# Kernel optimization log

Measured on AMD Instinct MI355X. Metric: run time of the kernel, lower is better.

The kernel has to match this reference:

```python
import jax, jax.numpy as jnp
import numpy as np

N_NODES = 100000
N_EDGES = 1600000
IN_DIM = 128
HIDDEN = 128


def setup_inputs() -> dict:
    key = jax.random.key(0)
    k1, k2, k3 = jax.random.split(key, 3)
    x = jax.random.normal(k1, (N_NODES, IN_DIM), dtype=jnp.float32)
    edge_index = jax.random.randint(k2, (2, N_EDGES), 0, N_NODES, dtype=jnp.int64)
    # Glorot-ish init for the GCN weight
    W = jax.random.normal(k3, (IN_DIM, HIDDEN), dtype=jnp.float32) * (1.0 / np.sqrt(IN_DIM))
    b = jnp.zeros((HIDDEN,), dtype=jnp.float32)
    return {"x": x, "edge_index": edge_index, "W": W, "b": b}


def reference(x, edge_index, W, b):
    N = x.shape[0]
    # PyG GCNConv: add self-loops, symmetric deg^{-1/2} normalization,
    # linear transform, scatter-add aggregation at destination, + bias.
    loop = jnp.arange(N, dtype=edge_index.dtype)
    src = jnp.concatenate([edge_index[0], loop])
    dst = jnp.concatenate([edge_index[1], loop])

    ones = jnp.ones(src.shape[0], dtype=x.dtype)
    deg = jax.ops.segment_sum(ones, dst, num_segments=N)  # in-degree incl. self-loop
    dinv = jnp.where(deg > 0, jax.lax.rsqrt(deg), 0.0)
    norm = dinv[src] * dinv[dst]  # [E+N]

    xw = x @ W  # [N, H] dense transform first (GCNConv default)
    msgs = xw[src] * norm[:, None]  # gather + scale, [E+N, H]
    out = jax.ops.segment_sum(msgs, dst, num_segments=N) + b  # scatter-add
    return jax.nn.relu(out)
```

## Files before the change

kernel.cpp:

```cpp
#include <hip/hip_runtime.h>
#include <hip/hip_bf16.h>


#define NP1 512
#define MAXB 1024

typedef short  short8 __attribute__((ext_vector_type(8)));
typedef float  f32x4  __attribute__((ext_vector_type(4)));

__device__ inline unsigned short f2b(float f) {
    unsigned u = __float_as_uint(f);
    return (unsigned short)((u + 0x7fffu + ((u >> 16) & 1u)) >> 16);
}

__device__ inline void acc4(float4& a, unsigned lo, unsigned hi) {
    a.x += __uint_as_float(lo << 16);
    a.y += __uint_as_float(lo & 0xffff0000u);
    a.z += __uint_as_float(hi << 16);
    a.w += __uint_as_float(hi & 0xffff0000u);
}

__global__ __launch_bounds__(256) void k_hist(const int* __restrict__ dst,
                                              int* __restrict__ hist,
                                              const float* __restrict__ W,
                                              unsigned short* __restrict__ Wt,
                                              int E, int B, int chunk) {
    __shared__ int h[MAXB];
    for (int i = threadIdx.x; i < B; i += 256) h[i] = 0;
    __syncthreads();
    int e0 = blockIdx.x * chunk;
    int e1 = min(E, e0 + chunk);
    for (int e = e0 + threadIdx.x; e < e1; e += 256)
        atomicAdd(&h[dst[e] >> 7], 1);
    __syncthreads();
    for (int i = threadIdx.x; i < B; i += 256)
        hist[i * NP1 + blockIdx.x] = h[i];
    if (blockIdx.x < 64) {
        int i = blockIdx.x * 256 + threadIdx.x;
        int k = i >> 7, n = i & 127;
        Wt[n * 128 + k] = f2b(W[k * 128 + n]);
    }
}

__global__ __launch_bounds__(256) void k_scanrow(int* __restrict__ hist,
                                                 int* __restrict__ btotal, int B) {
    __shared__ int s[256];
    const int b = blockIdx.x;
    const int t = threadIdx.x;
    int v0 = hist[b * NP1 + 2 * t];
    int v1 = hist[b * NP1 + 2 * t + 1];
    int pair = v0 + v1;
    s[t] = pair;
    __syncthreads();
    for (int off = 1; off < 256; off <<= 1) {
        int add = (t >= off) ? s[t - off] : 0;
        __syncthreads();
        s[t] += add;
        __syncthreads();
    }
    int exc = s[t] - pair;
    hist[b * NP1 + 2 * t]     = exc;
    hist[b * NP1 + 2 * t + 1] = exc + v0;
    if (t == 255) btotal[b] = s[255];
}

__global__ __launch_bounds__(256) void k_scanb(const int* __restrict__ btotal,
                                               int* __restrict__ bbase, int B) {
    __shared__ int s[256];
    const int t = threadIdx.x;
    int v[4];
    int loc = 0;
#pragma unroll
    for (int k = 0; k < 4; ++k) {
        int idx = t * 4 + k;
        v[k] = (idx < B) ? btotal[idx] : 0;
        loc += v[k];
    }
    s[t] = loc;
    __syncthreads();
    for (int off = 1; off < 256; off <<= 1) {
        int add = (t >= off) ? s[t - off] : 0;
        __syncthreads();
        s[t] += add;
        __syncthreads();
    }
    int run = s[t] - loc;
#pragma unroll
    for (int k = 0; k < 4; ++k) {
        int idx = t * 4 + k;
        if (idx < B) bbase[idx] = run;
        run += v[k];
    }
}

__global__ __launch_bounds__(256) void k_scatter(const int* __restrict__ src,
                                                 const int* __restrict__ dst,
                                                 const int* __restrict__ hist,
                                                 const int* __restrict__ bbase,
                                                 unsigned* __restrict__ bucketed,
                                                 int E, int B, int chunk) {
    __shared__ int cur[MAXB];
    for (int i = threadIdx.x; i < B; i += 256)
        cur[i] = bbase[i] + hist[i * NP1 + blockIdx.x];
    __syncthreads();
    int e0 = blockIdx.x * chunk;
    int e1 = min(E, e0 + chunk);
    for (int e = e0 + threadIdx.x; e < e1; e += 256) {
        int d = dst[e];
        int p = atomicAdd(&cur[d >> 7], 1);
        bucketed[p] = (unsigned)src[e] | ((unsigned)(d & 127) << 17);
    }
}

__global__ __launch_bounds__(256) void k_csr(const unsigned* __restrict__ bucketed,
                                             const int* __restrict__ bbase,
                                             const int* __restrict__ btotal,
                                             int* __restrict__ csr_src,
                                             int* __restrict__ rowptr,
                                             float* __restrict__ dinv_g,
                                             int E, int B, int N) {
    const int b = blockIdx.x;
    const int t = threadIdx.x;
    const int base = bbase[b];
    const int cnt = btotal[b];
    const int node0 = b << 7;

    __shared__ int sdeg[128], sscan[128], cur[128];
    if (t < 128) sdeg[t] = 0;
    __syncthreads();
    for (int i = t; i < cnt; i += 256)
        atomicAdd(&sdeg[bucketed[base + i] >> 17], 1);
    __syncthreads();
    if (t < 128) sscan[t] = sdeg[t];
    __syncthreads();
    for (int off = 1; off < 128; off <<= 1) {
        int add = 0;
        if (t < 128 && t >= off) add = sscan[t - off];
        __syncthreads();
        if (t < 128) sscan[t] += add;
        __syncthreads();
    }
    if (t < 128) {
        int rs = sscan[t] - sdeg[t];
        cur[t] = rs;
        int node = node0 + t;
        if (node < N) {
            rowptr[node] = base + rs;
            dinv_g[node] = rsqrtf((float)(sdeg[t] + 1));
        }
    }
    if (b == B - 1 && t == 0) rowptr[N] = E;
    __syncthreads();
    for (int i = t; i < cnt; i += 256) {
        unsigned w = bucketed[base + i];
        int p = atomicAdd(&cur[w >> 17], 1);
        csr_src[base + p] = (int)(w & 0x1FFFFu);
    }
}

__global__ __launch_bounds__(256) void k_gemm(const float* __restrict__ x,
                                              const unsigned short* __restrict__ Wt,
                                              const float* __restrict__ dinv,
                                              unsigned* __restrict__ xs_out,
                                              int N, int row_base) {
    __shared__ short out_lds[4][16][136];
    const int t = threadIdx.x;
    const int wv = t >> 6;
    const int lane = t & 63;
    const int quad = lane >> 4;
    const int lid = lane & 15;
    const int row0 = row_base + blockIdx.x * 64;

    int grow = row0 + wv * 16 + lid;
    int growc = grow < N ? grow : N - 1;
    short8 af[4];
#pragma unroll
    for (int q = 0; q < 4; ++q) {
        const float4* xr = (const float4*)(x + (size_t)growc * 128 + q * 32 + quad * 8);
        float4 f0 = xr[0], f1 = xr[1];
        af[q][0] = (short)f2b(f0.x); af[q][1] = (short)f2b(f0.y);
        af[q][2] = (short)f2b(f0.z); af[q][3] = (short)f2b(f0.w);
        af[q][4] = (short)f2b(f1.x); af[q][5] = (short)f2b(f1.y);
        af[q][6] = (short)f2b(f1.z); af[q][7] = (short)f2b(f1.w);
    }

    int drow = row0 + wv * 16 + quad * 4;
    float4 dv4;
    if (drow + 3 < N)      dv4 = *(const float4*)(dinv + drow);
    else {
        dv4.x = dinv[min(drow + 0, N - 1)];
        dv4.y = dinv[min(drow + 1, N - 1)];
        dv4.z = dinv[min(drow + 2, N - 1)];
        dv4.w = dinv[min(drow + 3, N - 1)];
    }

#pragma unroll
    for (int c = 0; c < 8; ++c) {
        f32x4 acc = {0.f, 0.f, 0.f, 0.f};
#pragma unroll
        for (int q = 0; q < 4; ++q) {
            const short8* bp = (const short8*)(Wt + (size_t)(c * 16 + lid) * 128 +
                                               q * 32 + quad * 8);
            acc = __builtin_amdgcn_mfma_f32_16x16x32_bf16(af[q], *bp, acc, 0, 0, 0);
        }
        out_lds[wv][quad * 4 + 0][c * 16 + lid] = (short)f2b(acc[0] * dv4.x);
        out_lds[wv][quad * 4 + 1][c * 16 + lid] = (short)f2b(acc[1] * dv4.y);
        out_lds[wv][quad * 4 + 2][c * 16 + lid] = (short)f2b(acc[2] * dv4.z);
        out_lds[wv][quad * 4 + 3][c * 16 + lid] = (short)f2b(acc[3] * dv4.w);
    }
    __syncthreads();

    int rl = lane >> 2;
    int cseg = lane & 3;
    int grow2 = row0 + wv * 16 + rl;
    if (grow2 <= N) {
        uint4* dstp = (uint4*)(xs_out + (size_t)grow2 * 64);
        if (grow2 < N) {
            const uint4* srcp = (const uint4*)((const char*)&out_lds[wv][rl][0] + cseg * 64);
#pragma unroll
            for (int tt = 0; tt < 4; ++tt) dstp[cseg * 4 + tt] = srcp[tt];
        } else {
            uint4 z = make_uint4(0u, 0u, 0u, 0u);
#pragma unroll
            for (int tt = 0; tt < 4; ++tt) dstp[cseg * 4 + tt] = z;
        }
    }
}

__global__ __launch_bounds__(256) void k_aggregate(const uint4* __restrict__ xs4,
                                                   const int* __restrict__ csr_src,
                                                   const int* __restrict__ rowptr,
                                                   const float* __restrict__ dinv,
                                                   const float* __restrict__ bias,
                                                   float* __restrict__ out,
                                                   int N, int n_begin, int n_end) {
    const int t = threadIdx.x;
    const int lane = t & 63;
    const int sub = lane & 15;
    const int gbase = lane & 48;
    const int n = n_begin + blockIdx.x * 16 + (t >> 4);
    if (n >= n_end) return;

    const int rs = rowptr[n];
    const int re = rowptr[n + 1];
    const float dv = dinv[n];
    const char* xb = (const char*)xs4;
    const unsigned subo = (unsigned)sub << 4;

    float4 a0 = make_float4(0.f, 0.f, 0.f, 0.f);
    float4 a1 = make_float4(0.f, 0.f, 0.f, 0.f);

    int idx = N;
    if (rs + sub < re) idx = csr_src[rs + sub];

    for (int i0 = rs; i0 < re; i0 += 16) {
        const int idx_cur = idx;
        const int i1 = i0 + 16;
        idx = N;
        if (i1 + sub < re) idx = csr_src[i1 + sub];
        int m = re - i0; if (m > 16) m = 16;

        {
            int r0 = __shfl(idx_cur, gbase + 0);
            int r1 = __shfl(idx_cur, gbase + 1);
            int r2 = __shfl(idx_cur, gbase + 2);
            int r3 = __shfl(idx_cur, gbase + 3);
            int r4 = __shfl(idx_cur, gbase + 4);
            int r5 = __shfl(idx_cur, gbase + 5);
            int r6 = __shfl(idx_cur, gbase + 6);
            int r7 = __shfl(idx_cur, gbase + 7);
            uint4 u0 = *(const uint4*)(xb + ((((unsigned)r0) << 8) | subo));
            uint4 u1 = *(const uint4*)(xb + ((((unsigned)r1) << 8) | subo));
            uint4 u2 = *(const uint4*)(xb + ((((unsigned)r2) << 8) | subo));
            uint4 u3 = *(const uint4*)(xb + ((((unsigned)r3) << 8) | subo));
            uint4 u4 = *(const uint4*)(xb + ((((unsigned)r4) << 8) | subo));
            uint4 u5 = *(const uint4*)(xb + ((((unsigned)r5) << 8) | subo));
            uint4 u6 = *(const uint4*)(xb + ((((unsigned)r6) << 8) | subo));
            uint4 u7 = *(const uint4*)(xb + ((((unsigned)r7) << 8) | subo));
            acc4(a0, u0.x, u0.y); acc4(a1, u0.z, u0.w);
            acc4(a0, u1.x, u1.y); acc4(a1, u1.z, u1.w);
            acc4(a0, u2.x, u2.y); acc4(a1, u2.z, u2.w);
            acc4(a0, u3.x, u3.y); acc4(a1, u3.z, u3.w);
            acc4(a0, u4.x, u4.y); acc4(a1, u4.z, u4.w);
            acc4(a0, u5.x, u5.y); acc4(a1, u5.z, u5.w);
            acc4(a0, u6.x, u6.y); acc4(a1, u6.z, u6.w);
            acc4(a0, u7.x, u7.y); acc4(a1, u7.z, u7.w);
        }
        if (m > 8) {
            int r0 = __shfl(idx_cur, gbase + 8);
            int r1 = __shfl(idx_cur, gbase + 9);
            int r2 = __shfl(idx_cur, gbase + 10);
            int r3 = __shfl(idx_cur, gbase + 11);
            int r4 = __shfl(idx_cur, gbase + 12);
            int r5 = __shfl(idx_cur, gbase + 13);
            int r6 = __shfl(idx_cur, gbase + 14);
            int r7 = __shfl(idx_cur, gbase + 15);
            uint4 u0 = *(const uint4*)(xb + ((((unsigned)r0) << 8) | subo));
            uint4 u1 = *(const uint4*)(xb + ((((unsigned)r1) << 8) | subo));
            uint4 u2 = *(const uint4*)(xb + ((((unsigned)r2) << 8) | subo));
            uint4 u3 = *(const uint4*)(xb + ((((unsigned)r3) << 8) | subo));
            uint4 u4 = *(const uint4*)(xb + ((((unsigned)r4) << 8) | subo));
            uint4 u5 = *(const uint4*)(xb + ((((unsigned)r5) << 8) | subo));
            uint4 u6 = *(const uint4*)(xb + ((((unsigned)r6) << 8) | subo));
            uint4 u7 = *(const uint4*)(xb + ((((unsigned)r7) << 8) | subo));
            acc4(a0, u0.x, u0.y); acc4(a1, u0.z, u0.w);
            acc4(a0, u1.x, u1.y); acc4(a1, u1.z, u1.w);
            acc4(a0, u2.x, u2.y); acc4(a1, u2.z, u2.w);
            acc4(a0, u3.x, u3.y); acc4(a1, u3.z, u3.w);
            acc4(a0, u4.x, u4.y); acc4(a1, u4.z, u4.w);
            acc4(a0, u5.x, u5.y); acc4(a1, u5.z, u5.w);
            acc4(a0, u6.x, u6.y); acc4(a1, u6.z, u6.w);
            acc4(a0, u7.x, u7.y); acc4(a1, u7.z, u7.w);
        }
    }

    uint4 su = *(const uint4*)(xb + ((((unsigned)n) << 8) | subo));
    acc4(a0, su.x, su.y);
    acc4(a1, su.z, su.w);

    const float4* bp = (const float4*)bias;
    float4 b0 = bp[sub * 2];
    float4 b1 = bp[sub * 2 + 1];
    f32x4 o0, o1;
    o0[0] = fmaxf(dv * a0.x + b0.x, 0.f);
    o0[1] = fmaxf(dv * a0.y + b0.y, 0.f);
    o0[2] = fmaxf(dv * a0.z + b0.z, 0.f);
    o0[3] = fmaxf(dv * a0.w + b0.w, 0.f);
    o1[0] = fmaxf(dv * a1.x + b1.x, 0.f);
    o1[1] = fmaxf(dv * a1.y + b1.y, 0.f);
    o1[2] = fmaxf(dv * a1.z + b1.z, 0.f);
    o1[3] = fmaxf(dv * a1.w + b1.w, 0.f);

    f32x4* op = (f32x4*)(out + (size_t)n * 128 + sub * 8);
    __builtin_nontemporal_store(o0, op);
    __builtin_nontemporal_store(o1, op + 1);
}

extern "C" void kernel_launch(void* const* d_in, const int* in_sizes, int n_in,
                              void* d_out, int out_size, void* d_ws, size_t ws_size,
                              hipStream_t stream) {
    const float* x   = (const float*)d_in[0];
    const int*   ei  = (const int*)d_in[1];
    const float* W   = (const float*)d_in[2];
    const float* b   = (const float*)d_in[3];
    float*       out = (float*)d_out;

    const int N = in_sizes[0] / 128;
    const int E = in_sizes[1] / 2;
    const int* src = ei;
    const int* dst = ei + E;

    const int B = (N + 127) >> 7;
    const int M = B * NP1;
    const int chunk = (E + NP1 - 1) / NP1;

    auto align = [](size_t v) { return (v + 255) & ~(size_t)255; };
    char* p = (char*)d_ws;
    int*            hist     = (int*)p;            p += align((size_t)M * 4);
    int*            btotal   = (int*)p;            p += align((size_t)B * 4);
    int*            bbase    = (int*)p;            p += align((size_t)B * 4);
    int*            rowptr   = (int*)p;            p += align(((size_t)N + 1) * 4);
    float*          dinv     = (float*)p;          p += align((size_t)N * 4);
    unsigned*       bucketed = (unsigned*)p;       p += align((size_t)E * 4);
    int*            csr_src  = (int*)p;            p += align((size_t)E * 4);
    unsigned*       xs       = (unsigned*)p;       p += align(((size_t)N + 1) * 64 * 4);
    unsigned short* Wt       = (unsigned short*)p; p += align(128 * 128 * 2);
    (void)ws_size;

    k_hist    <<<NP1, 256, 0, stream>>>(dst, hist, W, Wt, E, B, chunk);
    k_scanrow <<<B, 256, 0, stream>>>(hist, btotal, B);
    k_scanb   <<<1, 256, 0, stream>>>(btotal, bbase, B);
    k_scatter <<<NP1, 256, 0, stream>>>(src, dst, hist, bbase, bucketed, E, B, chunk);
    k_csr     <<<B, 256, 0, stream>>>(bucketed, bbase, btotal, csr_src, rowptr,
                                      dinv, E, B, N);

    const int half = ((N / 2) + 63) / 64 * 64;
    const int g1 = half / 64;
    const int g2 = (N + 1 - half + 63) / 64;
    k_gemm <<<g1, 256, 0, stream>>>(x, Wt, dinv, xs, N, 0);
    k_gemm <<<g2, 256, 0, stream>>>(x, Wt, dinv, xs, N, half);

    const int q = (N + 3) / 4;
    for (int i = 0; i < 4; ++i) {
        int n0 = i * q;
        int n1 = min(N, n0 + q);
        if (n0 >= n1) break;
        int blocks = (n1 - n0 + 15) / 16;
        k_aggregate<<<blocks, 256, 0, stream>>>((const uint4*)xs, csr_src, rowptr,
                                                dinv, b, out, N, n0, n1);
    }
}
```

Baseline: 258.7 us.

## Fold bucket-base scan into scatter/csr, widen buckets, merge gemm and aggregate launches

Removes the single-block bucket-total scan kernel and recomputes the bucket base prefix inside k_scatter and k_csr, so there is one fewer launch and dependency step. Bucket width grows from 128 to 256 nodes per bucket, which halves the bucket count and gives larger k_csr blocks. The two gemm launches become one, and the aggregate launches drop from four to two, cutting launch overhead. The cost is that every scatter and csr block now repeats a redundant 256-wide scan, and the 256-node buckets mean fewer csr blocks with more per-bucket LDS atomics.

```diff
diff --git a/kernel.cpp b/kernel.cpp
--- a/kernel.cpp
+++ b/kernel.cpp
@@ -3,7 +3,8 @@
 
 
 #define NP1 512
-#define MAXB 1024
+#define BSH 8
+#define MAXB 512
 
 typedef short  short8 __attribute__((ext_vector_type(8)));
 typedef float  f32x4  __attribute__((ext_vector_type(4)));
@@ -31,7 +32,7 @@
     int e0 = blockIdx.x * chunk;
     int e1 = min(E, e0 + chunk);
     for (int e = e0 + threadIdx.x; e < e1; e += 256)
-        atomicAdd(&h[dst[e] >> 7], 1);
+        atomicAdd(&h[dst[e] >> BSH], 1);
     __syncthreads();
     for (int i = threadIdx.x; i < B; i += 256)
         hist[i * NP1 + blockIdx.x] = h[i];
@@ -64,56 +65,41 @@
     if (t == 255) btotal[b] = s[255];
 }
 
-__global__ __launch_bounds__(256) void k_scanb(const int* __restrict__ btotal,
-                                               int* __restrict__ bbase, int B) {
-    __shared__ int s[256];
-    const int t = threadIdx.x;
-    int v[4];
-    int loc = 0;
-#pragma unroll
-    for (int k = 0; k < 4; ++k) {
-        int idx = t * 4 + k;
-        v[k] = (idx < B) ? btotal[idx] : 0;
-        loc += v[k];
-    }
-    s[t] = loc;
-    __syncthreads();
-    for (int off = 1; off < 256; off <<= 1) {
-        int add = (t >= off) ? s[t - off] : 0;
-        __syncthreads();
-        s[t] += add;
-        __syncthreads();
-    }
-    int run = s[t] - loc;
-#pragma unroll
-    for (int k = 0; k < 4; ++k) {
-        int idx = t * 4 + k;
-        if (idx < B) bbase[idx] = run;
-        run += v[k];
-    }
-}
-
 __global__ __launch_bounds__(256) void k_scatter(const int* __restrict__ src,
                                                  const int* __restrict__ dst,
                                                  const int* __restrict__ hist,
-                                                 const int* __restrict__ bbase,
+                                                 const int* __restrict__ btotal,
                                                  unsigned* __restrict__ bucketed,
                                                  int E, int B, int chunk) {
     __shared__ int cur[MAXB];
-    for (int i = threadIdx.x; i < B; i += 256)
-        cur[i] = bbase[i] + hist[i * NP1 + blockIdx.x];
-    __syncthreads();
-    int e0 = blockIdx.x * chunk;
+    __shared__ int s[256];
+    const int t = threadIdx.x;
+    const int g = blockIdx.x;
+    int a0 = (2 * t     < B) ? btotal[2 * t]     : 0;
+    int a1 = (2 * t + 1 < B) ? btotal[2 * t + 1] : 0;
+    int pair = a0 + a1;
+    s[t] = pair;
+    __syncthreads();
+    for (int off = 1; off < 256; off <<= 1) {
+        int add = (t >= off) ? s[t - off] : 0;
+        __syncthreads();
+        s[t] += add;
+        __syncthreads();
+    }
+    int ex = s[t] - pair;
+    if (2 * t     < B) cur[2 * t]     = ex      + hist[(2 * t)     * NP1 + g];
+    if (2 * t + 1 < B) cur[2 * t + 1] = ex + a0 + hist[(2 * t + 1) * NP1 + g];
+    __syncthreads();
+    int e0 = g * chunk;
     int e1 = min(E, e0 + chunk);
-    for (int e = e0 + threadIdx.x; e < e1; e += 256) {
+    for (int e = e0 + t; e < e1; e += 256) {
         int d = dst[e];
-        int p = atomicAdd(&cur[d >> 7], 1);
-        bucketed[p] = (unsigned)src[e] | ((unsigned)(d & 127) << 17);
+        int p = atomicAdd(&cur[d >> BSH], 1);
+        bucketed[p] = (unsigned)src[e] | ((unsigned)(d & 255) << 17);
     }
 }
 
 __global__ __launch_bounds__(256) void k_csr(const unsigned* __restrict__ bucketed,
-                                             const int* __restrict__ bbase,
                                              const int* __restrict__ btotal,
                                              int* __restrict__ csr_src,
                                              int* __restrict__ rowptr,
@@ -121,26 +107,42 @@
                                              int E, int B, int N) {
     const int b = blockIdx.x;
     const int t = threadIdx.x;
-    const int base = bbase[b];
+    __shared__ int sb[MAXB];
+    __shared__ int s[256];
+    __shared__ int sdeg[256], sscan[256], cur[256];
+    int a0 = (2 * t     < B) ? btotal[2 * t]     : 0;
+    int a1 = (2 * t + 1 < B) ? btotal[2 * t + 1] : 0;
+    int pair = a0 + a1;
+    s[t] = pair;
+    sdeg[t] = 0;
+    __syncthreads();
+    for (int off = 1; off < 256; off <<= 1) {
+        int add = (t >= off) ? s[t - off] : 0;
+        __syncthreads();
+        s[t] += add;
+        __syncthreads();
+    }
+    int ex = s[t] - pair;
+    if (2 * t     < B) sb[2 * t]     = ex;
+    if (2 * t + 1 < B) sb[2 * t + 1] = ex + a0;
+    __syncthreads();
+
+    const int base = sb[b];
     const int cnt = btotal[b];
-    const int node0 = b << 7;
-
-    __shared__ int sdeg[128], sscan[128], cur[128];
-    if (t < 128) sdeg[t] = 0;
-    __syncthreads();
+    const int node0 = b << BSH;
+
     for (int i = t; i < cnt; i += 256)
         atomicAdd(&sdeg[bucketed[base + i] >> 17], 1);
     __syncthreads();
-    if (t < 128) sscan[t] = sdeg[t];
-    __syncthreads();
-    for (int off = 1; off < 128; off <<= 1) {
-        int add = 0;
-        if (t < 128 && t >= off) add = sscan[t - off];
-        __syncthreads();
-        if (t < 128) sscan[t] += add;
-        __syncthreads();
-    }
-    if (t < 128) {
+    sscan[t] = sdeg[t];
+    __syncthreads();
+    for (int off = 1; off < 256; off <<= 1) {
+        int add = (t >= off) ? sscan[t - off] : 0;
+        __syncthreads();
+        sscan[t] += add;
+        __syncthreads();
+    }
+    {
         int rs = sscan[t] - sdeg[t];
         cur[t] = rs;
         int node = node0 + t;
@@ -161,15 +163,14 @@
 __global__ __launch_bounds__(256) void k_gemm(const float* __restrict__ x,
                                               const unsigned short* __restrict__ Wt,
                                               const float* __restrict__ dinv,
-                                              unsigned* __restrict__ xs_out,
-                                              int N, int row_base) {
+                                              unsigned* __restrict__ xs_out, int N) {
     __shared__ short out_lds[4][16][136];
     const int t = threadIdx.x;
     const int wv = t >> 6;
     const int lane = t & 63;
     const int quad = lane >> 4;
     const int lid = lane & 15;
-    const int row0 = row_base + blockIdx.x * 64;
+    const int row0 = blockIdx.x * 64;
 
     int grow = row0 + wv * 16 + lid;
     int growc = grow < N ? grow : N - 1;
@@ -350,7 +351,7 @@
     const int* src = ei;
     const int* dst = ei + E;
 
-    const int B = (N + 127) >> 7;
+    const int B = (N + 255) >> BSH;
     const int M = B * NP1;
     const int chunk = (E + NP1 - 1) / NP1;
 
@@ -358,7 +359,6 @@
     char* p = (char*)d_ws;
     int*            hist     = (int*)p;            p += align((size_t)M * 4);
     int*            btotal   = (int*)p;            p += align((size_t)B * 4);
-    int*            bbase    = (int*)p;            p += align((size_t)B * 4);
     int*            rowptr   = (int*)p;            p += align(((size_t)N + 1) * 4);
     float*          dinv     = (float*)p;          p += align((size_t)N * 4);
     unsigned*       bucketed = (unsigned*)p;       p += align((size_t)E * 4);
@@ -369,19 +369,13 @@
 
     k_hist    <<<NP1, 256, 0, stream>>>(dst, hist, W, Wt, E, B, chunk);
     k_scanrow <<<B, 256, 0, stream>>>(hist, btotal, B);
-    k_scanb   <<<1, 256, 0, stream>>>(btotal, bbase, B);
-    k_scatter <<<NP1, 256, 0, stream>>>(src, dst, hist, bbase, bucketed, E, B, chunk);
-    k_csr     <<<B, 256, 0, stream>>>(bucketed, bbase, btotal, csr_src, rowptr,
+    k_scatter <<<NP1, 256, 0, stream>>>(src, dst, hist, btotal, bucketed, E, B, chunk);
+    k_csr     <<<B, 256, 0, stream>>>(bucketed, btotal, csr_src, rowptr,
                                       dinv, E, B, N);
-
-    const int half = ((N / 2) + 63) / 64 * 64;
-    const int g1 = half / 64;
-    const int g2 = (N + 1 - half + 63) / 64;
-    k_gemm <<<g1, 256, 0, stream>>>(x, Wt, dinv, xs, N, 0);
-    k_gemm <<<g2, 256, 0, stream>>>(x, Wt, dinv, xs, N, half);
-
-    const int q = (N + 3) / 4;
-    for (int i = 0; i < 4; ++i) {
+    k_gemm    <<<N / 64 + 1, 256, 0, stream>>>(x, Wt, dinv, xs, N);
+
+    const int q = (N + 1) / 2;
+    for (int i = 0; i < 2; ++i) {
         int n0 = i * q;
         int n1 = min(N, n0 + q);
         if (n0 >= n1) break;
```

New measurement: 246.5 us. 4.7% less time.
